# Kernel optimization log

Hardware: AMD Instinct MI355X
Metric: run time of the kernel (lower is better)

Reference implementation:

```python
import jax, jax.numpy as jnp
import numpy as np

K = 2            # number of attention heads (k in __init__)
NEG = -9.0e15    # mask fill value from the torch code
N, C, CO = 6144, 128, 128


def _ln(x, g, b, eps=1e-5):
    m = x.mean(-1, keepdims=True)
    v = ((x - m) ** 2).mean(-1, keepdims=True)
    return (x - m) / jnp.sqrt(v + eps) * g + b


def setup_inputs() -> dict:
    key = jax.random.key(0)
    ks = jax.random.split(key, 6)
    x = jax.random.normal(ks[0], (N, C), jnp.float32)
    adj = (jax.random.uniform(ks[1], (N, N)) < 0.01).astype(jnp.float32)
    ff0_w = jax.random.normal(ks[2], (K, C, C), jnp.float32) / np.float32(np.sqrt(C))
    ff1_w = jax.random.normal(ks[3], (K, CO, C), jnp.float32) / np.float32(np.sqrt(C))
    attn_w = jax.random.normal(ks[4], (K, 2 * C), jnp.float32) / np.float32(np.sqrt(2 * C))
    return dict(
        x=x, adj=adj, ff0_w=ff0_w, ff1_w=ff1_w, attn_w=attn_w,
        g1=jnp.ones((C,), jnp.float32), b1=jnp.zeros((C,), jnp.float32),
        g2=jnp.ones((C,), jnp.float32), b2=jnp.zeros((C,), jnp.float32),
    )


def reference(x, adj, ff0_w, ff1_w, attn_w, g1, b1, g2, b2):
    n, c = x.shape
    co = ff1_w.shape[1]
    x_norm = _ln(x, g1, b1)
    # torch does adj = adj + eye(n) each iteration; since adj >= 0 the mask
    # (adj > 0) is identical for every iteration: original edges plus self-loops.
    mask = (adj > 0) | jnp.eye(n, dtype=bool)
    h_next = jnp.zeros((n, co), x.dtype)
    for i in range(K):  # small fixed head count, structurally distinct weights
        h = x_norm @ ff0_w[i].T  # [n, c]
        # attn_fc(cat(h_i, h_j)) == a1.h_i + a2.h_j  (exact decomposition of
        # the concat+linear; avoids materializing the [n, n, 2c] tensor)
        s_src = h @ attn_w[i, :c]  # [n], contribution of row node i
        s_dst = h @ attn_w[i, c:]  # [n], contribution of col node j
        e = jax.nn.leaky_relu(s_src[:, None] + s_dst[None, :])  # [n, n]
        e = jnp.where(mask, e, jnp.float32(NEG))
        atten = jax.nn.softmax(e, axis=1)  # dropout p=0.0 -> identity
        att = atten @ h + x  # residual adds pre-norm x
        att = _ln(att, g2, b2)
        h_next = h_next + jax.nn.elu(att @ ff1_w[i].T) / K
    return h_next
```

## Files before the change

kernel.cpp:

```cpp
#include <hip/hip_runtime.h>
#include <math.h>

#define Nn 6144
#define Cc 128
#define NHD 2
#define MAXDEG 192

__device__ __forceinline__ float wave_red_sum(float v) {
#pragma unroll
  for (int o = 32; o; o >>= 1) v += __shfl_xor(v, o);
  return v;
}

template <bool IS_MAX>
__device__ __forceinline__ void block_red2(float& a, float& b, float* red) {
#pragma unroll
  for (int o = 32; o; o >>= 1) {
    float ta = __shfl_xor(a, o), tb = __shfl_xor(b, o);
    if (IS_MAX) { a = fmaxf(a, ta); b = fmaxf(b, tb); }
    else        { a += ta;          b += tb;          }
  }
  int wid = threadIdx.x >> 6;
  __syncthreads();
  if ((threadIdx.x & 63) == 0) { red[wid] = a; red[4 + wid] = b; }
  __syncthreads();
  if (IS_MAX) {
    a = fmaxf(fmaxf(red[0], red[1]), fmaxf(red[2], red[3]));
    b = fmaxf(fmaxf(red[4], red[5]), fmaxf(red[6], red[7]));
  } else {
    a = red[0] + red[1] + red[2] + red[3];
    b = red[4] + red[5] + red[6] + red[7];
  }
}

__global__ __launch_bounds__(256) void k_ln(const float* __restrict__ x,
                                            const float* __restrict__ g,
                                            const float* __restrict__ b,
                                            float* __restrict__ xn) {
  int wid = threadIdx.x >> 6, lane = threadIdx.x & 63;
  int row = blockIdx.x * 4 + wid;
  float2 v = ((const float2*)(x + (size_t)row * Cc))[lane];
  float s = v.x + v.y;
#pragma unroll
  for (int o = 32; o; o >>= 1) s += __shfl_xor(s, o);
  float mean = s * (1.0f / Cc);
  float dx = v.x - mean, dy = v.y - mean;
  float q = dx * dx + dy * dy;
#pragma unroll
  for (int o = 32; o; o >>= 1) q += __shfl_xor(q, o);
  float rstd = rsqrtf(q * (1.0f / Cc) + 1e-5f);
  int c = lane * 2;
  float* o = xn + (size_t)row * Cc;
  o[c]     = dx * rstd * g[c] + b[c];
  o[c + 1] = dy * rstd * g[c + 1] + b[c + 1];
}

__global__ __launch_bounds__(256) void k_ff0(const float* __restrict__ A,
                                             const float* __restrict__ Bw,
                                             float* __restrict__ out) {
  __shared__ float As[64][68];
  __shared__ float Bs[64][132];
  const int t = threadIdx.x;
  const int head = blockIdx.y;
  const int row0 = blockIdx.x * 64;
  const float* Bh = Bw + (size_t)head * Cc * Cc;
  const int tr = t & 15, tc = t >> 4;
  const int r0 = tr * 4, c0 = tc * 8;
  float acc[4][8];
#pragma unroll
  for (int i = 0; i < 4; i++)
#pragma unroll
    for (int j = 0; j < 8; j++) acc[i][j] = 0.f;

  for (int kt = 0; kt < Cc; kt += 64) {
    __syncthreads();
    for (int i = t; i < 1024; i += 256) {
      int rr = i >> 4, k4 = i & 15;
      float4 v = *(const float4*)(A + (size_t)(row0 + rr) * Cc + kt + k4 * 4);
      As[k4 * 4 + 0][rr] = v.x; As[k4 * 4 + 1][rr] = v.y;
      As[k4 * 4 + 2][rr] = v.z; As[k4 * 4 + 3][rr] = v.w;
    }
    for (int i = t; i < 2048; i += 256) {
      int cc2 = i >> 4, k4 = i & 15;
      float4 v = *(const float4*)(Bh + (size_t)cc2 * Cc + kt + k4 * 4);
      Bs[k4 * 4 + 0][cc2] = v.x; Bs[k4 * 4 + 1][cc2] = v.y;
      Bs[k4 * 4 + 2][cc2] = v.z; Bs[k4 * 4 + 3][cc2] = v.w;
    }
    __syncthreads();
#pragma unroll
    for (int k = 0; k < 64; k++) {
      float4 a  = *(const float4*)&As[k][r0];
      float4 b0 = *(const float4*)&Bs[k][c0];
      float4 b1 = *(const float4*)&Bs[k][c0 + 4];
      float av[4] = {a.x, a.y, a.z, a.w};
      float bv[8] = {b0.x, b0.y, b0.z, b0.w, b1.x, b1.y, b1.z, b1.w};
#pragma unroll
      for (int i = 0; i < 4; i++)
#pragma unroll
        for (int j = 0; j < 8; j++) acc[i][j] = fmaf(av[i], bv[j], acc[i][j]);
    }
  }
#pragma unroll
  for (int i = 0; i < 4; i++) {
    float* op = out + ((size_t)head * Nn + row0 + r0 + i) * Cc + c0;
    *(float4*)(op)     = make_float4(acc[i][0], acc[i][1], acc[i][2], acc[i][3]);
    *(float4*)(op + 4) = make_float4(acc[i][4], acc[i][5], acc[i][6], acc[i][7]);
  }
}

__global__ __launch_bounds__(256) void k_attn_s(const float* __restrict__ h,
                                                const float* __restrict__ aw,
                                                float* __restrict__ ssrc,
                                                float* __restrict__ sdst) {
  int wid = threadIdx.x >> 6, lane = threadIdx.x & 63;
  int row = blockIdx.x * 4 + wid;
#pragma unroll
  for (int hd = 0; hd < NHD; hd++) {
    float2 v  = ((const float2*)(h + ((size_t)hd * Nn + row) * Cc))[lane];
    float2 w1 = ((const float2*)(aw + hd * 2 * Cc))[lane];
    float2 w2 = ((const float2*)(aw + hd * 2 * Cc + Cc))[lane];
    float a = v.x * w1.x + v.y * w1.y;
    float b = v.x * w2.x + v.y * w2.y;
#pragma unroll
    for (int o = 32; o; o >>= 1) { a += __shfl_xor(a, o); b += __shfl_xor(b, o); }
    if (lane == 0) { ssrc[hd * Nn + row] = a; sdst[hd * Nn + row] = b; }
  }
}

__global__ __launch_bounds__(256) void k_attn(
    const float* __restrict__ adj, const float* __restrict__ x,
    const float* __restrict__ h, const float* __restrict__ ssrc,
    const float* __restrict__ sdst, const float* __restrict__ g2,
    const float* __restrict__ b2, float* __restrict__ att_out) {
  __shared__ int nbr[MAXDEG];
  __shared__ float wts[NHD][MAXDEG];
  __shared__ float red[8];
  __shared__ int cnt;
  const int t = threadIdx.x;
  const int r = blockIdx.x;
  if (t == 0) cnt = 0;
  __syncthreads();
  const float4* arow = (const float4*)(adj + (size_t)r * Nn);
  for (int i = t; i < Nn / 4; i += 256) {
    float4 v = arow[i];
    int j = i * 4;
    if (v.x > 0.f || j + 0 == r) { int p = atomicAdd(&cnt, 1); if (p < MAXDEG) nbr[p] = j + 0; }
    if (v.y > 0.f || j + 1 == r) { int p = atomicAdd(&cnt, 1); if (p < MAXDEG) nbr[p] = j + 1; }
    if (v.z > 0.f || j + 2 == r) { int p = atomicAdd(&cnt, 1); if (p < MAXDEG) nbr[p] = j + 2; }
    if (v.w > 0.f || j + 3 == r) { int p = atomicAdd(&cnt, 1); if (p < MAXDEG) nbr[p] = j + 3; }
  }
  __syncthreads();
  const int deg = min(cnt, MAXDEG);
  float e0 = -3.0e38f, e1 = -3.0e38f;
  if (t < deg) {
    int j = nbr[t];
    e0 = ssrc[r] + sdst[j];
    e1 = ssrc[Nn + r] + sdst[Nn + j];
    e0 = (e0 > 0.f) ? e0 : 0.01f * e0;
    e1 = (e1 > 0.f) ? e1 : 0.01f * e1;
  }
  float m0 = e0, m1 = e1;
  block_red2<true>(m0, m1, red);
  float w0 = (t < deg) ? __expf(e0 - m0) : 0.f;
  float w1 = (t < deg) ? __expf(e1 - m1) : 0.f;
  float l0 = w0, l1 = w1;
  block_red2<false>(l0, l1, red);
  if (t < deg) { wts[0][t] = w0 / l0; wts[1][t] = w1 / l1; }
  __syncthreads();
  const int hd = t >> 7;
  const int c = t & 127;
  const float* hp = h + (size_t)hd * Nn * Cc + c;
  const float* wrow = wts[hd];
  float acc = 0.f;
  int k = 0;
  for (; k + 8 <= deg; k += 8) {
    int j0 = nbr[k],     j1 = nbr[k + 1], j2 = nbr[k + 2], j3 = nbr[k + 3];
    int j4 = nbr[k + 4], j5 = nbr[k + 5], j6 = nbr[k + 6], j7 = nbr[k + 7];
    float a0 = hp[(size_t)j0 * Cc], a1 = hp[(size_t)j1 * Cc];
    float a2 = hp[(size_t)j2 * Cc], a3 = hp[(size_t)j3 * Cc];
    float a4 = hp[(size_t)j4 * Cc], a5 = hp[(size_t)j5 * Cc];
    float a6 = hp[(size_t)j6 * Cc], a7 = hp[(size_t)j7 * Cc];
    acc = fmaf(wrow[k],     a0, acc); acc = fmaf(wrow[k + 1], a1, acc);
    acc = fmaf(wrow[k + 2], a2, acc); acc = fmaf(wrow[k + 3], a3, acc);
    acc = fmaf(wrow[k + 4], a4, acc); acc = fmaf(wrow[k + 5], a5, acc);
    acc = fmaf(wrow[k + 6], a6, acc); acc = fmaf(wrow[k + 7], a7, acc);
  }
  for (; k < deg; k++) acc = fmaf(wrow[k], hp[(size_t)nbr[k] * Cc], acc);
  float att = acc + x[(size_t)r * Cc + c];
  float s = wave_red_sum(att);
  int wid = t >> 6;
  __syncthreads();
  if ((t & 63) == 0) red[wid] = s;
  __syncthreads();
  float mean = (red[hd * 2] + red[hd * 2 + 1]) * (1.0f / Cc);
  float d = att - mean;
  float q = wave_red_sum(d * d);
  __syncthreads();
  if ((t & 63) == 0) red[wid] = q;
  __syncthreads();
  float var = (red[hd * 2] + red[hd * 2 + 1]) * (1.0f / Cc);
  float rstd = rsqrtf(var + 1e-5f);
  att_out[((size_t)hd * Nn + r) * Cc + c] = d * rstd * g2[c] + b2[c];
}

__global__ __launch_bounds__(256) void k_ff1(const float* __restrict__ A,
                                             const float* __restrict__ Bw,
                                             float* __restrict__ out) {
  __shared__ float As[64][68];
  __shared__ float Bs[64][132];
  const int t = threadIdx.x;
  const int row0 = blockIdx.x * 64;
  const int tr = t & 15, tc = t >> 4;
  const int r0 = tr * 4, c0 = tc * 8;
  float fin[4][8];
#pragma unroll
  for (int i = 0; i < 4; i++)
#pragma unroll
    for (int j = 0; j < 8; j++) fin[i][j] = 0.f;

  for (int head = 0; head < NHD; head++) {
    const float* Ah = A + (size_t)head * Nn * Cc;
    const float* Bh = Bw + (size_t)head * Cc * Cc;
    float acc[4][8];
#pragma unroll
    for (int i = 0; i < 4; i++)
#pragma unroll
      for (int j = 0; j < 8; j++) acc[i][j] = 0.f;
    for (int kt = 0; kt < Cc; kt += 64) {
      __syncthreads();
      for (int i = t; i < 1024; i += 256) {
        int rr = i >> 4, k4 = i & 15;
        float4 v = *(const float4*)(Ah + (size_t)(row0 + rr) * Cc + kt + k4 * 4);
        As[k4 * 4 + 0][rr] = v.x; As[k4 * 4 + 1][rr] = v.y;
        As[k4 * 4 + 2][rr] = v.z; As[k4 * 4 + 3][rr] = v.w;
      }
      for (int i = t; i < 2048; i += 256) {
        int cc2 = i >> 4, k4 = i & 15;
        float4 v = *(const float4*)(Bh + (size_t)cc2 * Cc + kt + k4 * 4);
        Bs[k4 * 4 + 0][cc2] = v.x; Bs[k4 * 4 + 1][cc2] = v.y;
        Bs[k4 * 4 + 2][cc2] = v.z; Bs[k4 * 4 + 3][cc2] = v.w;
      }
      __syncthreads();
#pragma unroll
      for (int k = 0; k < 64; k++) {
        float4 a  = *(const float4*)&As[k][r0];
        float4 b0 = *(const float4*)&Bs[k][c0];
        float4 b1 = *(const float4*)&Bs[k][c0 + 4];
        float av[4] = {a.x, a.y, a.z, a.w};
        float bv[8] = {b0.x, b0.y, b0.z, b0.w, b1.x, b1.y, b1.z, b1.w};
#pragma unroll
        for (int i = 0; i < 4; i++)
#pragma unroll
          for (int j = 0; j < 8; j++) acc[i][j] = fmaf(av[i], bv[j], acc[i][j]);
      }
    }
#pragma unroll
    for (int i = 0; i < 4; i++)
#pragma unroll
      for (int j = 0; j < 8; j++) {
        float v = acc[i][j];
        v = (v > 0.f) ? v : (expf(v) - 1.f);
        fin[i][j] += 0.5f * v;
      }
  }
#pragma unroll
  for (int i = 0; i < 4; i++) {
    float* op = out + (size_t)(row0 + r0 + i) * Cc + c0;
    *(float4*)(op)     = make_float4(fin[i][0], fin[i][1], fin[i][2], fin[i][3]);
    *(float4*)(op + 4) = make_float4(fin[i][4], fin[i][5], fin[i][6], fin[i][7]);
  }
}

extern "C" void kernel_launch(void* const* d_in, const int* in_sizes, int n_in,
                              void* d_out, int out_size, void* d_ws, size_t ws_size,
                              hipStream_t stream) {
  const float* x   = (const float*)d_in[0];
  const float* adj = (const float*)d_in[1];
  const float* ff0 = (const float*)d_in[2];
  const float* ff1 = (const float*)d_in[3];
  const float* aw  = (const float*)d_in[4];
  const float* g1  = (const float*)d_in[5];
  const float* b1  = (const float*)d_in[6];
  const float* g2  = (const float*)d_in[7];
  const float* b2  = (const float*)d_in[8];
  float* out = (float*)d_out;

  float* ws    = (float*)d_ws;
  float* xnorm = ws;
  float* h     = xnorm + (size_t)Nn * Cc;
  float* ssrc  = h + (size_t)2 * Nn * Cc;
  float* sdst  = ssrc + 2 * Nn;
  float* attn  = sdst + 2 * Nn;

  hipLaunchKernelGGL(k_ln, dim3(Nn / 4), dim3(256), 0, stream, x, g1, b1, xnorm);
  hipLaunchKernelGGL(k_ff0, dim3(Nn / 64, 2), dim3(256), 0, stream, xnorm, ff0, h);
  hipLaunchKernelGGL(k_attn_s, dim3(Nn / 4), dim3(256), 0, stream, h, aw, ssrc, sdst);
  hipLaunchKernelGGL(k_attn, dim3(Nn), dim3(256), 0, stream, adj, x, h, ssrc, sdst, g2, b2, attn);
  hipLaunchKernelGGL(k_ff1, dim3(Nn / 64), dim3(256), 0, stream, attn, ff1, out);
}
```

Baseline: 312.2 us.

## Split adjacency scan into ballot-based CSR kernel and shrink GEMM row tiles

The dense adjacency scan moves out of the attention kernel into its own kernel. There, one wave per row compacts the nonzero column indices in order, using ballot and popcount prefix sums instead of shared-memory atomics, and writes a padded neighbor list plus a degree to workspace. The attention kernel then only loads the precomputed list before computing softmax weights and gathering. Separately, the two GEMMs are merged into one template with 32-row tiles instead of 64, which doubles the block count. The trade-offs are an extra kernel launch and a global round-trip for the neighbor lists, and the list writes are not clamped at the 256-slot row capacity, so a row with higher degree would spill into the next row's slots.

```diff
diff --git a/kernel.cpp b/kernel.cpp
--- a/kernel.cpp
+++ b/kernel.cpp
@@ -4,7 +4,7 @@
 #define Nn 6144
 #define Cc 128
 #define NHD 2
-#define MAXDEG 192
+#define NBRS 256
 
 __device__ __forceinline__ float wave_red_sum(float v) {
 #pragma unroll
@@ -55,56 +55,85 @@
   o[c + 1] = dy * rstd * g[c + 1] + b[c + 1];
 }
 
-__global__ __launch_bounds__(256) void k_ff0(const float* __restrict__ A,
-                                             const float* __restrict__ Bw,
-                                             float* __restrict__ out) {
-  __shared__ float As[64][68];
+template <int MODE>
+__global__ __launch_bounds__(256) void k_gemm(const float* __restrict__ A,
+                                              const float* __restrict__ Bw,
+                                              float* __restrict__ out) {
+  __shared__ float As[64][34];
   __shared__ float Bs[64][132];
   const int t = threadIdx.x;
-  const int head = blockIdx.y;
-  const int row0 = blockIdx.x * 64;
-  const float* Bh = Bw + (size_t)head * Cc * Cc;
+  const int row0 = blockIdx.x * 32;
   const int tr = t & 15, tc = t >> 4;
-  const int r0 = tr * 4, c0 = tc * 8;
-  float acc[4][8];
-#pragma unroll
-  for (int i = 0; i < 4; i++)
-#pragma unroll
-    for (int j = 0; j < 8; j++) acc[i][j] = 0.f;
-
-  for (int kt = 0; kt < Cc; kt += 64) {
-    __syncthreads();
-    for (int i = t; i < 1024; i += 256) {
-      int rr = i >> 4, k4 = i & 15;
-      float4 v = *(const float4*)(A + (size_t)(row0 + rr) * Cc + kt + k4 * 4);
-      As[k4 * 4 + 0][rr] = v.x; As[k4 * 4 + 1][rr] = v.y;
-      As[k4 * 4 + 2][rr] = v.z; As[k4 * 4 + 3][rr] = v.w;
+  const int r0 = tr * 2, c0 = tc * 8;
+  float fin[2][8];
+#pragma unroll
+  for (int i = 0; i < 2; i++)
+#pragma unroll
+    for (int j = 0; j < 8; j++) fin[i][j] = 0.f;
+
+  const int h_begin = (MODE == 0) ? blockIdx.y : 0;
+  const int h_end   = (MODE == 0) ? blockIdx.y + 1 : NHD;
+  for (int head = h_begin; head < h_end; head++) {
+    const float* Ah = A + (MODE == 1 ? (size_t)head * Nn * Cc : (size_t)0);
+    const float* Bh = Bw + (size_t)head * Cc * Cc;
+    float acc[2][8];
+#pragma unroll
+    for (int i = 0; i < 2; i++)
+#pragma unroll
+      for (int j = 0; j < 8; j++) acc[i][j] = 0.f;
+    for (int kt = 0; kt < Cc; kt += 64) {
+      __syncthreads();
+      for (int i = t; i < 512; i += 256) {
+        int rr = i >> 4, k4 = i & 15;
+        float4 v = *(const float4*)(Ah + (size_t)(row0 + rr) * Cc + kt + k4 * 4);
+        As[k4 * 4 + 0][rr] = v.x; As[k4 * 4 + 1][rr] = v.y;
+        As[k4 * 4 + 2][rr] = v.z; As[k4 * 4 + 3][rr] = v.w;
+      }
+      for (int i = t; i < 2048; i += 256) {
+        int cc2 = i >> 4, k4 = i & 15;
+        float4 v = *(const float4*)(Bh + (size_t)cc2 * Cc + kt + k4 * 4);
+        Bs[k4 * 4 + 0][cc2] = v.x; Bs[k4 * 4 + 1][cc2] = v.y;
+        Bs[k4 * 4 + 2][cc2] = v.z; Bs[k4 * 4 + 3][cc2] = v.w;
+      }
+      __syncthreads();
+#pragma unroll
+      for (int k = 0; k < 64; k++) {
+        float2 a  = *(const float2*)&As[k][r0];
+        float4 b0 = *(const float4*)&Bs[k][c0];
+        float4 b1 = *(const float4*)&Bs[k][c0 + 4];
+        float av[2] = {a.x, a.y};
+        float bv[8] = {b0.x, b0.y, b0.z, b0.w, b1.x, b1.y, b1.z, b1.w};
+#pragma unroll
+        for (int i = 0; i < 2; i++)
+#pragma unroll
+          for (int j = 0; j < 8; j++) acc[i][j] = fmaf(av[i], bv[j], acc[i][j]);
+      }
     }
-    for (int i = t; i < 2048; i += 256) {
-      int cc2 = i >> 4, k4 = i & 15;
-      float4 v = *(const float4*)(Bh + (size_t)cc2 * Cc + kt + k4 * 4);
-      Bs[k4 * 4 + 0][cc2] = v.x; Bs[k4 * 4 + 1][cc2] = v.y;
-      Bs[k4 * 4 + 2][cc2] = v.z; Bs[k4 * 4 + 3][cc2] = v.w;
+    if (MODE == 0) {
+#pragma unroll
+      for (int i = 0; i < 2; i++) {
+        float* op = out + ((size_t)head * Nn + row0 + r0 + i) * Cc + c0;
+        *(float4*)(op)     = make_float4(acc[i][0], acc[i][1], acc[i][2], acc[i][3]);
+        *(float4*)(op + 4) = make_float4(acc[i][4], acc[i][5], acc[i][6], acc[i][7]);
+      }
+    } else {
+#pragma unroll
+      for (int i = 0; i < 2; i++)
+#pragma unroll
+        for (int j = 0; j < 8; j++) {
+          float v = acc[i][j];
+          v = (v > 0.f) ? v : (expf(v) - 1.f);
+          fin[i][j] += 0.5f * v;
+        }
     }
-    __syncthreads();
-#pragma unroll
-    for (int k = 0; k < 64; k++) {
-      float4 a  = *(const float4*)&As[k][r0];
-      float4 b0 = *(const float4*)&Bs[k][c0];
-      float4 b1 = *(const float4*)&Bs[k][c0 + 4];
-      float av[4] = {a.x, a.y, a.z, a.w};
-      float bv[8] = {b0.x, b0.y, b0.z, b0.w, b1.x, b1.y, b1.z, b1.w};
-#pragma unroll
-      for (int i = 0; i < 4; i++)
-#pragma unroll
-        for (int j = 0; j < 8; j++) acc[i][j] = fmaf(av[i], bv[j], acc[i][j]);
+  }
+  if (MODE == 1) {
+#pragma unroll
+    for (int i = 0; i < 2; i++) {
+      float* op = out + (size_t)(row0 + r0 + i) * Cc + c0;
+      *(float4*)(op)     = make_float4(fin[i][0], fin[i][1], fin[i][2], fin[i][3]);
+      *(float4*)(op + 4) = make_float4(fin[i][4], fin[i][5], fin[i][6], fin[i][7]);
     }
-  }
-#pragma unroll
-  for (int i = 0; i < 4; i++) {
-    float* op = out + ((size_t)head * Nn + row0 + r0 + i) * Cc + c0;
-    *(float4*)(op)     = make_float4(acc[i][0], acc[i][1], acc[i][2], acc[i][3]);
-    *(float4*)(op + 4) = make_float4(acc[i][4], acc[i][5], acc[i][6], acc[i][7]);
   }
 }
 
@@ -127,33 +156,53 @@
   }
 }
 
-__global__ __launch_bounds__(256) void k_attn(
-    const float* __restrict__ adj, const float* __restrict__ x,
-    const float* __restrict__ h, const float* __restrict__ ssrc,
-    const float* __restrict__ sdst, const float* __restrict__ g2,
-    const float* __restrict__ b2, float* __restrict__ att_out) {
-  __shared__ int nbr[MAXDEG];
-  __shared__ float wts[NHD][MAXDEG];
+__global__ __launch_bounds__(256) void k_csr(const float* __restrict__ adj,
+                                             int* __restrict__ nbr,
+                                             int* __restrict__ deg) {
+  const int lane = threadIdx.x & 63;
+  const int wid = threadIdx.x >> 6;
+  const int r = blockIdx.x * 4 + wid;
+  const float4* arow = (const float4*)(adj + (size_t)r * Nn);
+  int* nrow = nbr + (size_t)r * NBRS;
+  const unsigned long long ltmask = (1ull << lane) - 1ull;
+  int cnt = 0;
+  for (int i = lane; i < Nn / 4; i += 64) {
+    float4 v = arow[i];
+    int j = i * 4;
+    bool p0 = (v.x > 0.f) || (j + 0 == r);
+    bool p1 = (v.y > 0.f) || (j + 1 == r);
+    bool p2 = (v.z > 0.f) || (j + 2 == r);
+    bool p3 = (v.w > 0.f) || (j + 3 == r);
+    unsigned long long m0 = __ballot(p0);
+    unsigned long long m1 = __ballot(p1);
+    unsigned long long m2 = __ballot(p2);
+    unsigned long long m3 = __ballot(p3);
+    int c0 = __popcll(m0), c1 = __popcll(m1), c2 = __popcll(m2), c3 = __popcll(m3);
+    if (p0) nrow[cnt + __popcll(m0 & ltmask)] = j;
+    if (p1) nrow[cnt + c0 + __popcll(m1 & ltmask)] = j + 1;
+    if (p2) nrow[cnt + c0 + c1 + __popcll(m2 & ltmask)] = j + 2;
+    if (p3) nrow[cnt + c0 + c1 + c2 + __popcll(m3 & ltmask)] = j + 3;
+    cnt += c0 + c1 + c2 + c3;
+  }
+  if (lane == 0) deg[r] = cnt;
+}
+
+__global__ __launch_bounds__(256) void k_gather(
+    const int* __restrict__ nbr, const int* __restrict__ degp,
+    const float* __restrict__ x, const float* __restrict__ h,
+    const float* __restrict__ ssrc, const float* __restrict__ sdst,
+    const float* __restrict__ g2, const float* __restrict__ b2,
+    float* __restrict__ att_out) {
+  __shared__ int nbr_s[NBRS];
+  __shared__ float wts[NHD][NBRS];
   __shared__ float red[8];
-  __shared__ int cnt;
   const int t = threadIdx.x;
   const int r = blockIdx.x;
-  if (t == 0) cnt = 0;
-  __syncthreads();
-  const float4* arow = (const float4*)(adj + (size_t)r * Nn);
-  for (int i = t; i < Nn / 4; i += 256) {
-    float4 v = arow[i];
-    int j = i * 4;
-    if (v.x > 0.f || j + 0 == r) { int p = atomicAdd(&cnt, 1); if (p < MAXDEG) nbr[p] = j + 0; }
-    if (v.y > 0.f || j + 1 == r) { int p = atomicAdd(&cnt, 1); if (p < MAXDEG) nbr[p] = j + 1; }
-    if (v.z > 0.f || j + 2 == r) { int p = atomicAdd(&cnt, 1); if (p < MAXDEG) nbr[p] = j + 2; }
-    if (v.w > 0.f || j + 3 == r) { int p = atomicAdd(&cnt, 1); if (p < MAXDEG) nbr[p] = j + 3; }
-  }
-  __syncthreads();
-  const int deg = min(cnt, MAXDEG);
+  const int deg = min(degp[r], NBRS);
+  if (t < deg) nbr_s[t] = nbr[(size_t)r * NBRS + t];
   float e0 = -3.0e38f, e1 = -3.0e38f;
   if (t < deg) {
-    int j = nbr[t];
+    int j = nbr_s[t];
     e0 = ssrc[r] + sdst[j];
     e1 = ssrc[Nn + r] + sdst[Nn + j];
     e0 = (e0 > 0.f) ? e0 : 0.01f * e0;
@@ -174,8 +223,8 @@
   float acc = 0.f;
   int k = 0;
   for (; k + 8 <= deg; k += 8) {
-    int j0 = nbr[k],     j1 = nbr[k + 1], j2 = nbr[k + 2], j3 = nbr[k + 3];
-    int j4 = nbr[k + 4], j5 = nbr[k + 5], j6 = nbr[k + 6], j7 = nbr[k + 7];
+    int j0 = nbr_s[k],     j1 = nbr_s[k + 1], j2 = nbr_s[k + 2], j3 = nbr_s[k + 3];
+    int j4 = nbr_s[k + 4], j5 = nbr_s[k + 5], j6 = nbr_s[k + 6], j7 = nbr_s[k + 7];
     float a0 = hp[(size_t)j0 * Cc], a1 = hp[(size_t)j1 * Cc];
     float a2 = hp[(size_t)j2 * Cc], a3 = hp[(size_t)j3 * Cc];
     float a4 = hp[(size_t)j4 * Cc], a5 = hp[(size_t)j5 * Cc];
@@ -185,7 +234,7 @@
     acc = fmaf(wrow[k + 4], a4, acc); acc = fmaf(wrow[k + 5], a5, acc);
     acc = fmaf(wrow[k + 6], a6, acc); acc = fmaf(wrow[k + 7], a7, acc);
   }
-  for (; k < deg; k++) acc = fmaf(wrow[k], hp[(size_t)nbr[k] * Cc], acc);
+  for (; k < deg; k++) acc = fmaf(wrow[k], hp[(size_t)nbr_s[k] * Cc], acc);
   float att = acc + x[(size_t)r * Cc + c];
   float s = wave_red_sum(att);
   int wid = t >> 6;
@@ -201,74 +250,6 @@
   float var = (red[hd * 2] + red[hd * 2 + 1]) * (1.0f / Cc);
   float rstd = rsqrtf(var + 1e-5f);
   att_out[((size_t)hd * Nn + r) * Cc + c] = d * rstd * g2[c] + b2[c];
-}
-
-__global__ __launch_bounds__(256) void k_ff1(const float* __restrict__ A,
-                                             const float* __restrict__ Bw,
-                                             float* __restrict__ out) {
-  __shared__ float As[64][68];
-  __shared__ float Bs[64][132];
-  const int t = threadIdx.x;
-  const int row0 = blockIdx.x * 64;
-  const int tr = t & 15, tc = t >> 4;
-  const int r0 = tr * 4, c0 = tc * 8;
-  float fin[4][8];
-#pragma unroll
-  for (int i = 0; i < 4; i++)
-#pragma unroll
-    for (int j = 0; j < 8; j++) fin[i][j] = 0.f;
-
-  for (int head = 0; head < NHD; head++) {
-    const float* Ah = A + (size_t)head * Nn * Cc;
-    const float* Bh = Bw + (size_t)head * Cc * Cc;
-    float acc[4][8];
-#pragma unroll
-    for (int i = 0; i < 4; i++)
-#pragma unroll
-      for (int j = 0; j < 8; j++) acc[i][j] = 0.f;
-    for (int kt = 0; kt < Cc; kt += 64) {
-      __syncthreads();
-      for (int i = t; i < 1024; i += 256) {
-        int rr = i >> 4, k4 = i & 15;
-        float4 v = *(const float4*)(Ah + (size_t)(row0 + rr) * Cc + kt + k4 * 4);
-        As[k4 * 4 + 0][rr] = v.x; As[k4 * 4 + 1][rr] = v.y;
-        As[k4 * 4 + 2][rr] = v.z; As[k4 * 4 + 3][rr] = v.w;
-      }
-      for (int i = t; i < 2048; i += 256) {
-        int cc2 = i >> 4, k4 = i & 15;
-        float4 v = *(const float4*)(Bh + (size_t)cc2 * Cc + kt + k4 * 4);
-        Bs[k4 * 4 + 0][cc2] = v.x; Bs[k4 * 4 + 1][cc2] = v.y;
-        Bs[k4 * 4 + 2][cc2] = v.z; Bs[k4 * 4 + 3][cc2] = v.w;
-      }
-      __syncthreads();
-#pragma unroll
-      for (int k = 0; k < 64; k++) {
-        float4 a  = *(const float4*)&As[k][r0];
-        float4 b0 = *(const float4*)&Bs[k][c0];
-        float4 b1 = *(const float4*)&Bs[k][c0 + 4];
-        float av[4] = {a.x, a.y, a.z, a.w};
-        float bv[8] = {b0.x, b0.y, b0.z, b0.w, b1.x, b1.y, b1.z, b1.w};
-#pragma unroll
-        for (int i = 0; i < 4; i++)
-#pragma unroll
-          for (int j = 0; j < 8; j++) acc[i][j] = fmaf(av[i], bv[j], acc[i][j]);
-      }
-    }
-#pragma unroll
-    for (int i = 0; i < 4; i++)
-#pragma unroll
-      for (int j = 0; j < 8; j++) {
-        float v = acc[i][j];
-        v = (v > 0.f) ? v : (expf(v) - 1.f);
-        fin[i][j] += 0.5f * v;
-      }
-  }
-#pragma unroll
-  for (int i = 0; i < 4; i++) {
-    float* op = out + (size_t)(row0 + r0 + i) * Cc + c0;
-    *(float4*)(op)     = make_float4(fin[i][0], fin[i][1], fin[i][2], fin[i][3]);
-    *(float4*)(op + 4) = make_float4(fin[i][4], fin[i][5], fin[i][6], fin[i][7]);
-  }
 }
 
 extern "C" void kernel_launch(void* const* d_in, const int* in_sizes, int n_in,
@@ -291,10 +272,14 @@
   float* ssrc  = h + (size_t)2 * Nn * Cc;
   float* sdst  = ssrc + 2 * Nn;
   float* attn  = sdst + 2 * Nn;
+  int*   nbr   = (int*)(attn + (size_t)2 * Nn * Cc);
+  int*   deg   = nbr + (size_t)Nn * NBRS;
 
   hipLaunchKernelGGL(k_ln, dim3(Nn / 4), dim3(256), 0, stream, x, g1, b1, xnorm);
-  hipLaunchKernelGGL(k_ff0, dim3(Nn / 64, 2), dim3(256), 0, stream, xnorm, ff0, h);
+  hipLaunchKernelGGL((k_gemm<0>), dim3(Nn / 32, 2), dim3(256), 0, stream, xnorm, ff0, h);
   hipLaunchKernelGGL(k_attn_s, dim3(Nn / 4), dim3(256), 0, stream, h, aw, ssrc, sdst);
-  hipLaunchKernelGGL(k_attn, dim3(Nn), dim3(256), 0, stream, adj, x, h, ssrc, sdst, g2, b2, attn);
-  hipLaunchKernelGGL(k_ff1, dim3(Nn / 64), dim3(256), 0, stream, attn, ff1, out);
-}
+  hipLaunchKernelGGL(k_csr, dim3(Nn / 4), dim3(256), 0, stream, adj, nbr, deg);
+  hipLaunchKernelGGL(k_gather, dim3(Nn), dim3(256), 0, stream,
+                     nbr, deg, x, h, ssrc, sdst, g2, b2, attn);
+  hipLaunchKernelGGL((k_gemm<1>), dim3(Nn / 32), dim3(256), 0, stream, attn, ff1, out);
+}
```

After: 317.4 us. Within noise of the previous version (+1.7%).
